# Kernel optimization log

Measured on AMD Instinct MI355X. Metric: run time of the kernel, lower is better.

The kernel has to match this reference:

```python
import jax, jax.numpy as jnp
import numpy as np

B, T, D = 64, 2048, 256

def setup_inputs() -> dict:
    key = jax.random.key(0)
    k1, _ = jax.random.split(key)
    ts = jnp.arange(T, dtype=jnp.float32) * 0.01  # increasing time grid
    noise = jax.random.normal(k1, (B, T, D), dtype=jnp.float32)
    mu = jnp.zeros((D,), jnp.float32)
    log_kappa = jnp.full((D,), -0.7, jnp.float32)
    log_sigma = jnp.full((D,), -0.7, jnp.float32)
    return {"ts": ts, "noise": noise, "mu": mu, "log_kappa": log_kappa, "log_sigma": log_sigma}

def _A_Q(kappa, sigma, dt):
    # exact OU transition coefficients; dt: [T-1,1], kappa/sigma: [D] -> [T-1,D]
    A = jnp.exp(-kappa * dt)
    two_k_dt = 2.0 * kappa * dt
    small = (two_k_dt < 1e-6).astype(dt.dtype)
    Q_exact = sigma ** 2 * (1.0 - jnp.exp(-two_k_dt)) / jnp.maximum(2.0 * kappa, 1e-12)
    Q_taylor = sigma ** 2 * dt * (1.0 - kappa * dt + two_k_dt ** 2 / 6.0)
    Q = small * Q_taylor + (1.0 - small) * Q_exact
    return A, Q

def reference(ts, noise, mu, log_kappa, log_sigma):
    kappa = jax.nn.softplus(log_kappa) + 1e-6
    sigma = jax.nn.softplus(log_sigma) + 1e-6
    var0 = sigma ** 2 / (2.0 * kappa)                      # stationary variance [D]
    y0 = mu + noise[:, 0, :] * jnp.sqrt(var0)              # [B,D]
    dt = jnp.maximum(ts[1:] - ts[:-1], 1e-6)[:, None]      # [T-1,1]
    A, Q = _A_Q(kappa, sigma, dt)                          # [T-1,D]
    # mean = mu + A*(y-mu) = A*y + mu*(1-A); fold noise in ahead of the scan
    b = mu * (1.0 - A)                                     # [T-1,D]
    eps = jnp.swapaxes(noise[:, 1:, :], 0, 1) * jnp.sqrt(Q)[:, None, :]  # [T-1,B,D]

    def step(y, xs):
        A_k, b_k, e_k = xs
        y_new = A_k * y + b_k + e_k
        return y_new, y_new

    _, ys = jax.lax.scan(step, y0, (A, b, eps))            # [T-1,B,D]
    y = jnp.concatenate([y0[None], ys], axis=0)            # [T,B,D]
    return jnp.swapaxes(y, 0, 1)                           # [B,T,D]
```

## Files before the change

### kernel.cpp

```cpp
#include <hip/hip_runtime.h>
#include <math.h>

#define BB 64
#define TT 2048
#define DD 256
#define D4 64
#define SS 64
#define LL (TT / SS)
#define WPB 4
#define BPG (BB / WPB)
#define GRID (SS * BPG)

typedef float f4 __attribute__((ext_vector_type(4)));


__device__ __forceinline__ float softplus_f(float x) {
    return (x > 0.f) ? (x + log1pf(expf(-x))) : log1pf(expf(x));
}

struct P4 { f4 k, s2, r, mu; };
struct C4 { f4 A, bm, sQ; };
struct P1 { float k, s2, r; };
struct C1 { float A, bm, sQ; };

__device__ __forceinline__ P1 sp1(float lk, float ls) {
    P1 o;
    o.k = softplus_f(lk) + 1e-6f;
    float s = softplus_f(ls) + 1e-6f;
    o.s2 = s * s;
    o.r = o.s2 / fmaxf(2.f * o.k, 1e-12f);
    return o;
}

__device__ __forceinline__ P4 load_params4(const f4* __restrict__ mu4,
                                           const f4* __restrict__ lk4,
                                           const f4* __restrict__ ls4,
                                           int lane) {
    f4 lk = lk4[lane], ls = ls4[lane], mu = mu4[lane];
    P4 p;
    P1 a;
    a = sp1(lk.x, ls.x); p.k.x = a.k; p.s2.x = a.s2; p.r.x = a.r;
    a = sp1(lk.y, ls.y); p.k.y = a.k; p.s2.y = a.s2; p.r.y = a.r;
    a = sp1(lk.z, ls.z); p.k.z = a.k; p.s2.z = a.s2; p.r.z = a.r;
    a = sp1(lk.w, ls.w); p.k.w = a.k; p.s2.w = a.s2; p.r.w = a.r;
    p.mu = mu;
    return p;
}

__device__ __forceinline__ C1 ou_coeff(float dt, float kappa, float s2, float r,
                                       float mu) {
    C1 o;
    float e = kappa * dt;
    o.A = __expf(-e);
    float two = 2.f * e;
    float Qe = r * (1.f - o.A * o.A);
    float Qt = s2 * dt * fmaf(two * two, (1.f / 6.f), 1.f - e);
    float Q = (two < 1e-6f) ? Qt : Qe;
    o.sQ = sqrtf(Q);
    o.bm = mu * (1.f - o.A);
    return o;
}

__device__ __forceinline__ C4 coeff4(float dt, const P4& p) {
    C4 c;
    C1 o;
    o = ou_coeff(dt, p.k.x, p.s2.x, p.r.x, p.mu.x); c.A.x = o.A; c.bm.x = o.bm; c.sQ.x = o.sQ;
    o = ou_coeff(dt, p.k.y, p.s2.y, p.r.y, p.mu.y); c.A.y = o.A; c.bm.y = o.bm; c.sQ.y = o.sQ;
    o = ou_coeff(dt, p.k.z, p.s2.z, p.r.z, p.mu.z); c.A.z = o.A; c.bm.z = o.bm; c.sQ.z = o.sQ;
    o = ou_coeff(dt, p.k.w, p.s2.w, p.r.w, p.mu.w); c.A.w = o.A; c.bm.w = o.bm; c.sQ.w = o.sQ;
    return c;
}

__device__ __forceinline__ void ou_step4(const C4& cc, const f4 n, f4& y) {
    f4 cv = cc.sQ * n + cc.bm;
    y = cc.A * y + cv;
}

__device__ __forceinline__ f4 sqrt4(const f4 v) {
    f4 r;
    r.x = sqrtf(v.x); r.y = sqrtf(v.y); r.z = sqrtf(v.z); r.w = sqrtf(v.w);
    return r;
}

__global__ __launch_bounds__(256) void ou_partials(
    const float* __restrict__ ts, const f4* __restrict__ noise4,
    const f4* __restrict__ mu4, const f4* __restrict__ lk4,
    const f4* __restrict__ ls4,
    f4* __restrict__ Pw, f4* __restrict__ Uw) {
    __shared__ float dts[LL];
    const int lane = threadIdx.x & 63;
    const int w = threadIdx.x >> 6;
    const int s = blockIdx.x / BPG;
    const int bg = blockIdx.x % BPG;
    const int b = bg * WPB + w;
    const int t0 = s * LL;

    if (threadIdx.x < LL) {
        int k = t0 + threadIdx.x;
        float dt = 1e-6f;
        if (k >= 1) dt = fmaxf(ts[k] - ts[k - 1], 1e-6f);
        dts[threadIdx.x] = dt;
    }
    __syncthreads();

    P4 p = load_params4(mu4, lk4, ls4, lane);
    const f4* np = noise4 + (size_t)b * TT * D4 + lane;

    f4 U = {0.f, 0.f, 0.f, 0.f};
    f4 P = {1.f, 1.f, 1.f, 1.f};
    int kstart = t0;
    if (s == 0) {
        f4 n0 = np[0];
        U = n0 * sqrt4(p.r) + p.mu;
        P = (f4){0.f, 0.f, 0.f, 0.f};
        kstart = 1;
    }

    float dtprev = -1.f;
    C4 cc;
#pragma unroll 4
    for (int k = kstart; k < t0 + LL; ++k) {
        float dt = dts[k - t0];
        f4 n = np[(size_t)k * D4];
        if (dt != dtprev) { cc = coeff4(dt, p); dtprev = dt; }
        ou_step4(cc, n, U);
        P *= cc.A;
    }

    size_t idx = ((size_t)s * BB + b) * D4 + lane;
    Pw[idx] = P;
    Uw[idx] = U;
}

__global__ __launch_bounds__(256) void ou_scan_replay(
    const float* __restrict__ ts, const f4* __restrict__ noise4,
    const f4* __restrict__ mu4, const f4* __restrict__ lk4,
    const f4* __restrict__ ls4,
    const f4* __restrict__ Pw, const f4* __restrict__ Uw,
    f4* __restrict__ out4) {
    __shared__ float dts[LL];
    const int lane = threadIdx.x & 63;
    const int w = threadIdx.x >> 6;
    const int s = (SS - 1) - (blockIdx.x / BPG);
    const int bg = blockIdx.x % BPG;
    const int b = bg * WPB + w;
    const int t0 = s * LL;

    if (threadIdx.x < LL) {
        int k = t0 + threadIdx.x;
        float dt = 1e-6f;
        if (k >= 1) dt = fmaxf(ts[k] - ts[k - 1], 1e-6f);
        dts[threadIdx.x] = dt;
    }
    __syncthreads();

    P4 p = load_params4(mu4, lk4, ls4, lane);
    const f4* np = noise4 + (size_t)b * TT * D4 + lane;
    f4* op = out4 + (size_t)b * TT * D4 + lane;

    f4 y;
    int kstart = t0;
    if (s == 0) {
        f4 n0 = np[0];
        y = n0 * sqrt4(p.r) + p.mu;
        __builtin_nontemporal_store(y, op);
        kstart = 1;
    } else {
        const size_t stride = (size_t)BB * D4;
        const size_t i0 = (size_t)b * D4 + lane;
        f4 inc = Uw[i0];
#pragma unroll 4
        for (int j = 1; j < s; ++j) {
            size_t idx = i0 + (size_t)j * stride;
            f4 Pv = Pw[idx];
            f4 Uv = Uw[idx];
            inc = Pv * inc + Uv;
        }
        y = inc;
    }

    float dtprev = -1.f;
    C4 cc;
#pragma unroll 4
    for (int k = kstart; k < t0 + LL; ++k) {
        float dt = dts[k - t0];
        f4 n = np[(size_t)k * D4];
        if (dt != dtprev) { cc = coeff4(dt, p); dtprev = dt; }
        ou_step4(cc, n, y);
        __builtin_nontemporal_store(y, op + (size_t)k * D4);
    }
}

__global__ __launch_bounds__(128) void ou_fallback(
    const float* __restrict__ ts, const float2* __restrict__ noise2,
    const float2* __restrict__ mu2, const float2* __restrict__ lk2,
    const float2* __restrict__ ls2, float2* __restrict__ out2) {
    __shared__ float dts[TT];
    const int tid = threadIdx.x;
    const int b = blockIdx.x;
    for (int i = tid; i < TT; i += 128) {
        float dt = 1e-6f;
        if (i >= 1) dt = fmaxf(ts[i] - ts[i - 1], 1e-6f);
        dts[i] = dt;
    }
    __syncthreads();

    float2 lk = lk2[tid], ls = ls2[tid], mu = mu2[tid];
    P1 px = sp1(lk.x, ls.x);
    P1 py = sp1(lk.y, ls.y);

    const float2* np = noise2 + (size_t)b * TT * 128 + tid;
    float2* op = out2 + (size_t)b * TT * 128 + tid;

    float2 n0 = np[0];
    float2 y;
    y.x = fmaf(n0.x, sqrtf(px.r), mu.x);
    y.y = fmaf(n0.y, sqrtf(py.r), mu.y);
    op[0] = y;

#pragma unroll 4
    for (int k = 1; k < TT; ++k) {
        float dt = dts[k];
        float2 n = np[(size_t)k * 128];
        C1 cx = ou_coeff(dt, px.k, px.s2, px.r, mu.x);
        C1 cy = ou_coeff(dt, py.k, py.s2, py.r, mu.y);
        y.x = fmaf(cx.A, y.x, fmaf(cx.sQ, n.x, cx.bm));
        y.y = fmaf(cy.A, y.y, fmaf(cy.sQ, n.y, cy.bm));
        op[(size_t)k * 128] = y;
    }
}

extern "C" void kernel_launch(void* const* d_in, const int* in_sizes, int n_in,
                              void* d_out, int out_size, void* d_ws, size_t ws_size,
                              hipStream_t stream) {
    const float* ts = (const float*)d_in[0];
    const f4* noise4 = (const f4*)d_in[1];
    const f4* mu4 = (const f4*)d_in[2];
    const f4* lk4 = (const f4*)d_in[3];
    const f4* ls4 = (const f4*)d_in[4];
    f4* out4 = (f4*)d_out;

    const size_t seg = (size_t)SS * BB * D4;
    if (ws_size >= 2 * seg * sizeof(f4)) {
        f4* Pw = (f4*)d_ws;
        f4* Uw = Pw + seg;
        ou_partials<<<GRID, 256, 0, stream>>>(ts, noise4, mu4, lk4, ls4, Pw, Uw);
        ou_scan_replay<<<GRID, 256, 0, stream>>>(ts, noise4, mu4, lk4, ls4,
                                                 Pw, Uw, out4);
    } else {
        ou_fallback<<<BB, 128, 0, stream>>>(ts, (const float2*)d_in[1],
                                            (const float2*)d_in[2],
                                            (const float2*)d_in[3],
                                            (const float2*)d_in[4],
                                            (float2*)d_out);
    }
}
```

Baseline: 88.86 us.

## Double segment count, interleave P/U workspace, swap nontemporal loads and stores

Raises the number of time segments from 64 to 128, which doubles the grid and halves the serial chunk length per thread. P and U partials are now stored interleaved in one workspace array. Noise reads become nontemporal loads and output writes become ordinary stores, so the output may stay in cache. In exchange, each replay block does a longer serial carry-in scan over prior segments and the workspace traffic doubles.

```diff
diff --git a/kernel.cpp b/kernel.cpp
--- a/kernel.cpp
+++ b/kernel.cpp
@@ -3,9 +3,8 @@
 
 #define BB 64
 #define TT 2048
-#define DD 256
 #define D4 64
-#define SS 64
+#define SS 128
 #define LL (TT / SS)
 #define WPB 4
 #define BPG (BB / WPB)
@@ -71,11 +70,6 @@
     return c;
 }
 
-__device__ __forceinline__ void ou_step4(const C4& cc, const f4 n, f4& y) {
-    f4 cv = cc.sQ * n + cc.bm;
-    y = cc.A * y + cv;
-}
-
 __device__ __forceinline__ f4 sqrt4(const f4 v) {
     f4 r;
     r.x = sqrtf(v.x); r.y = sqrtf(v.y); r.z = sqrtf(v.z); r.w = sqrtf(v.w);
@@ -86,7 +80,7 @@
     const float* __restrict__ ts, const f4* __restrict__ noise4,
     const f4* __restrict__ mu4, const f4* __restrict__ lk4,
     const f4* __restrict__ ls4,
-    f4* __restrict__ Pw, f4* __restrict__ Uw) {
+    f4* __restrict__ PU) {
     __shared__ float dts[LL];
     const int lane = threadIdx.x & 63;
     const int w = threadIdx.x >> 6;
@@ -110,7 +104,7 @@
     f4 P = {1.f, 1.f, 1.f, 1.f};
     int kstart = t0;
     if (s == 0) {
-        f4 n0 = np[0];
+        f4 n0 = __builtin_nontemporal_load(np);
         U = n0 * sqrt4(p.r) + p.mu;
         P = (f4){0.f, 0.f, 0.f, 0.f};
         kstart = 1;
@@ -121,23 +115,23 @@
 #pragma unroll 4
     for (int k = kstart; k < t0 + LL; ++k) {
         float dt = dts[k - t0];
-        f4 n = np[(size_t)k * D4];
+        f4 n = __builtin_nontemporal_load(np + (size_t)k * D4);
         if (dt != dtprev) { cc = coeff4(dt, p); dtprev = dt; }
-        ou_step4(cc, n, U);
+        f4 cv = cc.sQ * n + cc.bm;
+        U = cc.A * U + cv;
         P *= cc.A;
     }
 
-    size_t idx = ((size_t)s * BB + b) * D4 + lane;
-    Pw[idx] = P;
-    Uw[idx] = U;
+    size_t base = (((size_t)s * BB + b) * D4 + lane) * 2;
+    PU[base] = P;
+    PU[base + 1] = U;
 }
 
 __global__ __launch_bounds__(256) void ou_scan_replay(
     const float* __restrict__ ts, const f4* __restrict__ noise4,
     const f4* __restrict__ mu4, const f4* __restrict__ lk4,
     const f4* __restrict__ ls4,
-    const f4* __restrict__ Pw, const f4* __restrict__ Uw,
-    f4* __restrict__ out4) {
+    const f4* __restrict__ PU, f4* __restrict__ out4) {
     __shared__ float dts[LL];
     const int lane = threadIdx.x & 63;
     const int w = threadIdx.x >> 6;
@@ -161,19 +155,19 @@
     f4 y;
     int kstart = t0;
     if (s == 0) {
-        f4 n0 = np[0];
+        f4 n0 = __builtin_nontemporal_load(np);
         y = n0 * sqrt4(p.r) + p.mu;
-        __builtin_nontemporal_store(y, op);
+        op[0] = y;
         kstart = 1;
     } else {
+        f4 inc = {0.f, 0.f, 0.f, 0.f};
+        const size_t lbase = (size_t)b * D4 + lane;
         const size_t stride = (size_t)BB * D4;
-        const size_t i0 = (size_t)b * D4 + lane;
-        f4 inc = Uw[i0];
-#pragma unroll 4
-        for (int j = 1; j < s; ++j) {
-            size_t idx = i0 + (size_t)j * stride;
-            f4 Pv = Pw[idx];
-            f4 Uv = Uw[idx];
+#pragma unroll 4
+        for (int j = 0; j < s; ++j) {
+            size_t base = (lbase + (size_t)j * stride) * 2;
+            f4 Pv = PU[base];
+            f4 Uv = PU[base + 1];
             inc = Pv * inc + Uv;
         }
         y = inc;
@@ -184,10 +178,11 @@
 #pragma unroll 4
     for (int k = kstart; k < t0 + LL; ++k) {
         float dt = dts[k - t0];
-        f4 n = np[(size_t)k * D4];
+        f4 n = __builtin_nontemporal_load(np + (size_t)k * D4);
         if (dt != dtprev) { cc = coeff4(dt, p); dtprev = dt; }
-        ou_step4(cc, n, y);
-        __builtin_nontemporal_store(y, op + (size_t)k * D4);
+        f4 cv = cc.sQ * n + cc.bm;
+        y = cc.A * y + cv;
+        op[(size_t)k * D4] = y;
     }
 }
 
@@ -240,13 +235,12 @@
     const f4* ls4 = (const f4*)d_in[4];
     f4* out4 = (f4*)d_out;
 
-    const size_t seg = (size_t)SS * BB * D4;
-    if (ws_size >= 2 * seg * sizeof(f4)) {
-        f4* Pw = (f4*)d_ws;
-        f4* Uw = Pw + seg;
-        ou_partials<<<GRID, 256, 0, stream>>>(ts, noise4, mu4, lk4, ls4, Pw, Uw);
+    const size_t need = (size_t)SS * BB * D4 * 2 * sizeof(f4);
+    if (ws_size >= need) {
+        f4* PU = (f4*)d_ws;
+        ou_partials<<<GRID, 256, 0, stream>>>(ts, noise4, mu4, lk4, ls4, PU);
         ou_scan_replay<<<GRID, 256, 0, stream>>>(ts, noise4, mu4, lk4, ls4,
-                                                 Pw, Uw, out4);
+                                                 PU, out4);
     } else {
         ou_fallback<<<BB, 128, 0, stream>>>(ts, (const float2*)d_in[1],
                                             (const float2*)d_in[2],
```

Result: slower. 135.6 us (+52.6%).
